# Kernel optimization log

Measured on AMD Instinct MI355X. Metric: run time of the kernel, lower is better.

The kernel has to match this reference:

```python
import jax, jax.numpy as jnp
import numpy as np

ALPHA = 0.2  # LeakyReLU negative slope


def setup_inputs() -> dict:
    key = jax.random.key(0)
    k1, k2, k3, k4 = jax.random.split(key, 4)
    B, W, N = 128, 128, 512  # batch, window_size, n_features
    x = jax.random.normal(k1, (B, W, N), dtype=jnp.float32)
    W_fc = jax.random.normal(k2, (W, W), dtype=jnp.float32) * (1.0 / np.sqrt(W))
    b_fc = jax.random.normal(k3, (W,), dtype=jnp.float32) * 0.01
    attn = jax.random.normal(k4, (2 * W, 1), dtype=jnp.float32) * (1.414 / np.sqrt(2 * W))
    return {"x": x, "W_fc": W_fc, "b_fc": b_fc, "attn": attn}


def reference(x, W_fc, b_fc, attn):
    # x: (B, window_size, n_features)
    Wsz = attn.shape[0] // 2
    xp = jnp.transpose(x, (0, 2, 1))                 # (B, N, W)
    h = jnp.einsum('bnw,vw->bnv', xp, W_fc) + b_fc   # fc over window dim: (B, N, W)
    # Split-projection equivalent of concat([x_i, h_j]) @ attn:
    a1 = attn[:Wsz, 0]
    a2 = attn[Wsz:, 0]
    s1 = xp @ a1                                     # (B, N) -- x_i part (repeat_interleave)
    s2 = h @ a2                                      # (B, N) -- h_j part (repeat)
    e = jax.nn.leaky_relu(s1[:, :, None] + s2[:, None, :], negative_slope=ALPHA)  # (B, N, N)
    attention = jax.nn.softmax(e, axis=2)            # softmax over j
    # dropout is identity in eval mode (train=False)
    out = jax.nn.sigmoid(jnp.einsum('bij,bjw->biw', attention, xp))  # (B, N, W)
    return jnp.transpose(out, (0, 2, 1))             # (B, W, N)
```

## Files before the change

kernel.cpp:

```cpp
#include <hip/hip_runtime.h>

#define Bb 128
#define Ww 128
#define Nn 512
#define ALPHA 0.2f
#define LOG2E 1.44269504088896340736f

typedef __attribute__((ext_vector_type(8))) short short8;
typedef __attribute__((ext_vector_type(4))) float f32x4;

__device__ __forceinline__ unsigned pk_bf16(float lo, float hi) {
  unsigned r;
  asm("v_cvt_pk_bf16_f32 %0, %1, %2" : "=v"(r) : "v"(lo), "v"(hi));
  return r;
}

__device__ __forceinline__ float v_exp2(float x) {
  float r;
  asm("v_exp_f32 %0, %1" : "=v"(r) : "v"(x));
  return r;
}

__device__ __forceinline__ float v_rcp(float x) {
  float r;
  asm("v_rcp_f32 %0, %1" : "=v"(r) : "v"(x));
  return r;
}

#define T_OFF   0
#define T_BYTES (64 * 129 * 8 * 2)
#define SR_OFF  (T_OFF + T_BYTES)
#define S1_OFF  (SR_OFF + 16384)
#define S2_OFF  (S1_OFF + 2048)
#define CV_OFF  (S2_OFF + 2048)
#define SMEM11  (CV_OFF + 528)

__launch_bounds__(512, 1)
__global__ void attn_f9(const float* __restrict__ x, const float* __restrict__ Wfc,
                        const float* __restrict__ bfc, const float* __restrict__ attn,
                        float* __restrict__ out) {
  extern __shared__ char smem[];
  ushort* tile = (ushort*)(smem + T_OFF);
  float*  sred = (float*)(smem + SR_OFF);
  float*  s1s  = (float*)(smem + S1_OFF);
  float*  s2s  = (float*)(smem + S2_OFF);
  float*  cvs  = (float*)(smem + CV_OFF);

  const int bid = blockIdx.x;
  const int xcd = bid & 7, idx = bid >> 3;
  const int b  = xcd * 16 + (idx >> 1);
  const int i0 = (idx & 1) * 256;
  const int t  = threadIdx.x;
  const int wv = t >> 6, lane = t & 63;
  const int wl = lane & 15, lg = lane >> 4;
  const float* xb = x + (size_t)b * (Ww * Nn);
  const int q = t & 63;

  {
    const int wcol = t & 127, vq = t >> 7;
    float p = 0.f;
#pragma unroll 8
    for (int vi = 0; vi < 32; ++vi) {
      const int v = vq * 32 + vi;
      p = fmaf(attn[Ww + v], Wfc[v * Ww + wcol], p);
    }
    sred[t] = p;
    if (t < 64) {
      float c0p = fmaf(bfc[t], attn[Ww + t], bfc[t + 64] * attn[Ww + 64 + t]);
#pragma unroll
      for (int off = 32; off; off >>= 1) c0p += __shfl_xor(c0p, off);
      if (t == 0) cvs[Ww] = c0p;
    }
  }
  __syncthreads();
  if (t < Ww) cvs[t] = sred[t] + sred[t + 128] + sred[t + 256] + sred[t + 384];
  __syncthreads();

  float s1p[8] = {0, 0, 0, 0, 0, 0, 0, 0};
  float s2p[8] = {0, 0, 0, 0, 0, 0, 0, 0};
  {
    float4 L0[16], L1[16];
#pragma unroll
    for (int k = 0; k < 16; ++k) {
      const float* s = xb + (size_t)(wv + 8 * k) * Nn + 8 * q;
      L0[k] = *reinterpret_cast<const float4*>(s);
      L1[k] = *reinterpret_cast<const float4*>(s + 4);
    }
#pragma unroll
    for (int k = 0; k < 16; ++k) {
      const int w = wv + 8 * k;
      const float aw = attn[w];
      const float cw = cvs[w];
      const float4 lo = L0[k], hi = L1[k];
      s1p[0] = fmaf(lo.x, aw, s1p[0]); s1p[1] = fmaf(lo.y, aw, s1p[1]);
      s1p[2] = fmaf(lo.z, aw, s1p[2]); s1p[3] = fmaf(lo.w, aw, s1p[3]);
      s1p[4] = fmaf(hi.x, aw, s1p[4]); s1p[5] = fmaf(hi.y, aw, s1p[5]);
      s1p[6] = fmaf(hi.z, aw, s1p[6]); s1p[7] = fmaf(hi.w, aw, s1p[7]);
      s2p[0] = fmaf(lo.x, cw, s2p[0]); s2p[1] = fmaf(lo.y, cw, s2p[1]);
      s2p[2] = fmaf(lo.z, cw, s2p[2]); s2p[3] = fmaf(lo.w, cw, s2p[3]);
      s2p[4] = fmaf(hi.x, cw, s2p[4]); s2p[5] = fmaf(hi.y, cw, s2p[5]);
      s2p[6] = fmaf(hi.z, cw, s2p[6]); s2p[7] = fmaf(hi.w, cw, s2p[7]);
      uint4 pk;
      pk.x = pk_bf16(lo.x, lo.y); pk.y = pk_bf16(lo.z, lo.w);
      pk.z = pk_bf16(hi.x, hi.y); pk.w = pk_bf16(hi.z, hi.w);
      *reinterpret_cast<uint4*>(tile + ((size_t)q * 129 + w) * 8) = pk;
    }
  }

  {
    f32x4* sv = reinterpret_cast<f32x4*>(&sred[t * 8]);
    sv[0] = (f32x4){s1p[0], s1p[1], s1p[2], s1p[3]};
    sv[1] = (f32x4){s1p[4], s1p[5], s1p[6], s1p[7]};
  }
  __syncthreads();
  float red;
  {
    float a = 0.f;
#pragma unroll
    for (int g = 0; g < 8; ++g) a += sred[((g * 64) + (t >> 3)) * 8 + (t & 7)];
    red = a;
  }
  __syncthreads();
  {
    s1s[t] = red * LOG2E;
    f32x4* sv = reinterpret_cast<f32x4*>(&sred[t * 8]);
    sv[0] = (f32x4){s2p[0], s2p[1], s2p[2], s2p[3]};
    sv[1] = (f32x4){s2p[4], s2p[5], s2p[6], s2p[7]};
  }
  __syncthreads();
  {
    float d = 0.f;
#pragma unroll
    for (int g = 0; g < 8; ++g) d += sred[((g * 64) + (t >> 3)) * 8 + (t & 7)];
    s2s[t] = (d + cvs[Ww]) * LOG2E;
  }
  __syncthreads();

  float s1i[2];
  s1i[0] = s1s[i0 + wv * 32 + wl];
  s1i[1] = s1s[i0 + wv * 32 + 16 + wl];

  f32x4 acc[2][8];
  f32x4 accl[2];
#pragma unroll
  for (int a = 0; a < 2; ++a) {
    accl[a] = (f32x4){0.f, 0.f, 0.f, 0.f};
#pragma unroll
    for (int f = 0; f < 8; ++f) acc[a][f] = (f32x4){0.f, 0.f, 0.f, 0.f};
  }
  short8 ones;
#pragma unroll
  for (int e = 0; e < 8; ++e) ones[e] = (short)0x3F80;

  for (int jj = 0; jj < 16; ++jj) {
    const int jb = jj * 32 + 8 * lg;
    float sv[8];
    *reinterpret_cast<float4*>(&sv[0]) = *reinterpret_cast<const float4*>(&s2s[jb]);
    *reinterpret_cast<float4*>(&sv[4]) = *reinterpret_cast<const float4*>(&s2s[jb + 4]);
    float p0[8], p1[8];
#pragma unroll
    for (int e = 0; e < 8; ++e) {
      const float u0 = s1i[0] + sv[e];
      p0[e] = v_exp2(fmaxf(u0, ALPHA * u0));
      const float u1 = s1i[1] + sv[e];
      p1[e] = v_exp2(fmaxf(u1, ALPHA * u1));
    }
    short8 af0, af1;
    unsigned* a0u = reinterpret_cast<unsigned*>(&af0);
    unsigned* a1u = reinterpret_cast<unsigned*>(&af1);
    a0u[0] = pk_bf16(p0[0], p0[1]); a0u[1] = pk_bf16(p0[2], p0[3]);
    a0u[2] = pk_bf16(p0[4], p0[5]); a0u[3] = pk_bf16(p0[6], p0[7]);
    a1u[0] = pk_bf16(p1[0], p1[1]); a1u[1] = pk_bf16(p1[2], p1[3]);
    a1u[2] = pk_bf16(p1[4], p1[5]); a1u[3] = pk_bf16(p1[6], p1[7]);

    const ushort* tb = tile + (size_t)(jj * 4 + lg) * 129 * 8;
#pragma unroll
    for (int f = 0; f < 8; ++f) {
      const short8 bfr = *reinterpret_cast<const short8*>(tb + (16 * f + wl) * 8);
      acc[0][f] = __builtin_amdgcn_mfma_f32_16x16x32_bf16(af0, bfr, acc[0][f], 0, 0, 0);
      acc[1][f] = __builtin_amdgcn_mfma_f32_16x16x32_bf16(af1, bfr, acc[1][f], 0, 0, 0);
    }
    accl[0] = __builtin_amdgcn_mfma_f32_16x16x32_bf16(af0, ones, accl[0], 0, 0, 0);
    accl[1] = __builtin_amdgcn_mfma_f32_16x16x32_bf16(af1, ones, accl[1], 0, 0, 0);
  }

  float* outb = out + (size_t)b * (Ww * Nn);
#pragma unroll
  for (int a = 0; a < 2; ++a) {
    float invl[4];
#pragma unroll
    for (int m = 0; m < 4; ++m) invl[m] = LOG2E * v_rcp(accl[a][m]);
    const int ibase = i0 + wv * 32 + 16 * a + lg * 4;
#pragma unroll
    for (int f = 0; f < 8; ++f) {
      float4 o;
      o.x = v_rcp(1.f + v_exp2(-(acc[a][f][0] * invl[0])));
      o.y = v_rcp(1.f + v_exp2(-(acc[a][f][1] * invl[1])));
      o.z = v_rcp(1.f + v_exp2(-(acc[a][f][2] * invl[2])));
      o.w = v_rcp(1.f + v_exp2(-(acc[a][f][3] * invl[3])));
      *reinterpret_cast<float4*>(outb + (16 * f + wl) * Nn + ibase) = o;
    }
  }
}

extern "C" void kernel_launch(void* const* d_in, const int* in_sizes, int n_in,
                              void* d_out, int out_size, void* d_ws, size_t ws_size,
                              hipStream_t stream) {
  const float* x    = (const float*)d_in[0];
  const float* Wfc  = (const float*)d_in[1];
  const float* bfc  = (const float*)d_in[2];
  const float* attn = (const float*)d_in[3];
  float* out = (float*)d_out;

  (void)hipFuncSetAttribute(reinterpret_cast<const void*>(&attn_f9),
                            hipFuncAttributeMaxDynamicSharedMemorySize, SMEM11);
  attn_f9<<<256, 512, SMEM11, stream>>>(x, Wfc, bfc, attn, out);
}
```

Baseline: 28.07 us.

## Double block size to 1024 threads, one 16-row tile per wave

The block grows from 8 to 16 waves. Each wave now computes a single 16-row MFMA tile instead of two, and the staging, transposition and reduction phases are re-split so each thread loads one float4 per row instead of two. The aim is more wave-level parallelism and latency hiding per CU, plus fewer registers per thread. The cost is more barrier participants, half the A-fragment reuse per LDS B-fragment load (doubling LDS read traffic), and 8-byte instead of 16-byte tile writes.

Result: faster. 26.38 us (-6.0%).

```diff
diff --git a/kernel.cpp b/kernel.cpp
--- a/kernel.cpp
+++ b/kernel.cpp
@@ -33,12 +33,12 @@
 #define S1_OFF  (SR_OFF + 16384)
 #define S2_OFF  (S1_OFF + 2048)
 #define CV_OFF  (S2_OFF + 2048)
-#define SMEM11  (CV_OFF + 528)
+#define SMEM12  (CV_OFF + 528)
 
-__launch_bounds__(512, 1)
-__global__ void attn_f9(const float* __restrict__ x, const float* __restrict__ Wfc,
-                        const float* __restrict__ bfc, const float* __restrict__ attn,
-                        float* __restrict__ out) {
+__launch_bounds__(1024, 1)
+__global__ void attn_k(const float* __restrict__ x, const float* __restrict__ Wfc,
+                       const float* __restrict__ bfc, const float* __restrict__ attn,
+                       float* __restrict__ out) {
   extern __shared__ char smem[];
   ushort* tile = (ushort*)(smem + T_OFF);
   float*  sred = (float*)(smem + SR_OFF);
@@ -51,17 +51,19 @@
   const int b  = xcd * 16 + (idx >> 1);
   const int i0 = (idx & 1) * 256;
   const int t  = threadIdx.x;
-  const int wv = t >> 6, lane = t & 63;
+  const int wvw = t >> 6;
+  const int lane = t & 63;
   const int wl = lane & 15, lg = lane >> 4;
+  const int g  = t >> 7;
+  const int q2 = t & 127;
   const float* xb = x + (size_t)b * (Ww * Nn);
-  const int q = t & 63;
 
   {
     const int wcol = t & 127, vq = t >> 7;
     float p = 0.f;
-#pragma unroll 8
-    for (int vi = 0; vi < 32; ++vi) {
-      const int v = vq * 32 + vi;
+#pragma unroll
+    for (int vi = 0; vi < 16; ++vi) {
+      const int v = vq * 16 + vi;
       p = fmaf(attn[Ww + v], Wfc[v * Ww + wcol], p);
     }
     sred[t] = p;
@@ -73,81 +75,63 @@
     }
   }
   __syncthreads();
-  if (t < Ww) cvs[t] = sred[t] + sred[t + 128] + sred[t + 256] + sred[t + 384];
+  if (t < Ww) {
+    float s = 0.f;
+#pragma unroll
+    for (int j = 0; j < 8; ++j) s += sred[t + 128 * j];
+    cvs[t] = s;
+  }
   __syncthreads();
 
-  float s1p[8] = {0, 0, 0, 0, 0, 0, 0, 0};
-  float s2p[8] = {0, 0, 0, 0, 0, 0, 0, 0};
+  float s1p[4] = {0.f, 0.f, 0.f, 0.f};
+  float s2p[4] = {0.f, 0.f, 0.f, 0.f};
   {
-    float4 L0[16], L1[16];
+    float4 L[16];
+#pragma unroll
+    for (int k = 0; k < 16; ++k)
+      L[k] = *reinterpret_cast<const float4*>(xb + (size_t)(g + 8 * k) * Nn + 4 * q2);
 #pragma unroll
     for (int k = 0; k < 16; ++k) {
-      const float* s = xb + (size_t)(wv + 8 * k) * Nn + 8 * q;
-      L0[k] = *reinterpret_cast<const float4*>(s);
-      L1[k] = *reinterpret_cast<const float4*>(s + 4);
-    }
-#pragma unroll
-    for (int k = 0; k < 16; ++k) {
-      const int w = wv + 8 * k;
+      const int w = g + 8 * k;
       const float aw = attn[w];
       const float cw = cvs[w];
-      const float4 lo = L0[k], hi = L1[k];
-      s1p[0] = fmaf(lo.x, aw, s1p[0]); s1p[1] = fmaf(lo.y, aw, s1p[1]);
-      s1p[2] = fmaf(lo.z, aw, s1p[2]); s1p[3] = fmaf(lo.w, aw, s1p[3]);
-      s1p[4] = fmaf(hi.x, aw, s1p[4]); s1p[5] = fmaf(hi.y, aw, s1p[5]);
-      s1p[6] = fmaf(hi.z, aw, s1p[6]); s1p[7] = fmaf(hi.w, aw, s1p[7]);
-      s2p[0] = fmaf(lo.x, cw, s2p[0]); s2p[1] = fmaf(lo.y, cw, s2p[1]);
-      s2p[2] = fmaf(lo.z, cw, s2p[2]); s2p[3] = fmaf(lo.w, cw, s2p[3]);
-      s2p[4] = fmaf(hi.x, cw, s2p[4]); s2p[5] = fmaf(hi.y, cw, s2p[5]);
-      s2p[6] = fmaf(hi.z, cw, s2p[6]); s2p[7] = fmaf(hi.w, cw, s2p[7]);
-      uint4 pk;
-      pk.x = pk_bf16(lo.x, lo.y); pk.y = pk_bf16(lo.z, lo.w);
-      pk.z = pk_bf16(hi.x, hi.y); pk.w = pk_bf16(hi.z, hi.w);
-      *reinterpret_cast<uint4*>(tile + ((size_t)q * 129 + w) * 8) = pk;
+      const float4 v = L[k];
+      s1p[0] = fmaf(v.x, aw, s1p[0]); s1p[1] = fmaf(v.y, aw, s1p[1]);
+      s1p[2] = fmaf(v.z, aw, s1p[2]); s1p[3] = fmaf(v.w, aw, s1p[3]);
+      s2p[0] = fmaf(v.x, cw, s2p[0]); s2p[1] = fmaf(v.y, cw, s2p[1]);
+      s2p[2] = fmaf(v.z, cw, s2p[2]); s2p[3] = fmaf(v.w, cw, s2p[3]);
+      uint2 pk;
+      pk.x = pk_bf16(v.x, v.y);
+      pk.y = pk_bf16(v.z, v.w);
+      *reinterpret_cast<uint2*>(tile + ((size_t)(q2 >> 1) * 129 + w) * 8 + (q2 & 1) * 4) = pk;
     }
   }
 
-  {
-    f32x4* sv = reinterpret_cast<f32x4*>(&sred[t * 8]);
-    sv[0] = (f32x4){s1p[0], s1p[1], s1p[2], s1p[3]};
-    sv[1] = (f32x4){s1p[4], s1p[5], s1p[6], s1p[7]};
+  *reinterpret_cast<f32x4*>(&sred[t * 4]) = (f32x4){s1p[0], s1p[1], s1p[2], s1p[3]};
+  __syncthreads();
+  float red = 0.f;
+  if (t < 512) {
+#pragma unroll
+    for (int j = 0; j < 8; ++j) red += sred[j * 512 + t];
   }
   __syncthreads();
-  float red;
-  {
-    float a = 0.f;
-#pragma unroll
-    for (int g = 0; g < 8; ++g) a += sred[((g * 64) + (t >> 3)) * 8 + (t & 7)];
-    red = a;
-  }
+  if (t < 512) s1s[t] = red * LOG2E;
+  *reinterpret_cast<f32x4*>(&sred[t * 4]) = (f32x4){s2p[0], s2p[1], s2p[2], s2p[3]};
   __syncthreads();
-  {
-    s1s[t] = red * LOG2E;
-    f32x4* sv = reinterpret_cast<f32x4*>(&sred[t * 8]);
-    sv[0] = (f32x4){s2p[0], s2p[1], s2p[2], s2p[3]};
-    sv[1] = (f32x4){s2p[4], s2p[5], s2p[6], s2p[7]};
-  }
-  __syncthreads();
-  {
+  if (t < 512) {
     float d = 0.f;
 #pragma unroll
-    for (int g = 0; g < 8; ++g) d += sred[((g * 64) + (t >> 3)) * 8 + (t & 7)];
+    for (int j = 0; j < 8; ++j) d += sred[j * 512 + t];
     s2s[t] = (d + cvs[Ww]) * LOG2E;
   }
   __syncthreads();
 
-  float s1i[2];
-  s1i[0] = s1s[i0 + wv * 32 + wl];
-  s1i[1] = s1s[i0 + wv * 32 + 16 + wl];
+  const float s1i = s1s[i0 + wvw * 16 + wl];
 
-  f32x4 acc[2][8];
-  f32x4 accl[2];
+  f32x4 acc[8];
+  f32x4 accl = (f32x4){0.f, 0.f, 0.f, 0.f};
 #pragma unroll
-  for (int a = 0; a < 2; ++a) {
-    accl[a] = (f32x4){0.f, 0.f, 0.f, 0.f};
-#pragma unroll
-    for (int f = 0; f < 8; ++f) acc[a][f] = (f32x4){0.f, 0.f, 0.f, 0.f};
-  }
+  for (int f = 0; f < 8; ++f) acc[f] = (f32x4){0.f, 0.f, 0.f, 0.f};
   short8 ones;
 #pragma unroll
   for (int e = 0; e < 8; ++e) ones[e] = (short)0x3F80;
@@ -157,49 +141,39 @@
     float sv[8];
     *reinterpret_cast<float4*>(&sv[0]) = *reinterpret_cast<const float4*>(&s2s[jb]);
     *reinterpret_cast<float4*>(&sv[4]) = *reinterpret_cast<const float4*>(&s2s[jb + 4]);
-    float p0[8], p1[8];
+    float p[8];
 #pragma unroll
     for (int e = 0; e < 8; ++e) {
-      const float u0 = s1i[0] + sv[e];
-      p0[e] = v_exp2(fmaxf(u0, ALPHA * u0));
-      const float u1 = s1i[1] + sv[e];
-      p1[e] = v_exp2(fmaxf(u1, ALPHA * u1));
+      const float u = s1i + sv[e];
+      p[e] = v_exp2(fmaxf(u, ALPHA * u));
     }
-    short8 af0, af1;
-    unsigned* a0u = reinterpret_cast<unsigned*>(&af0);
-    unsigned* a1u = reinterpret_cast<unsigned*>(&af1);
-    a0u[0] = pk_bf16(p0[0], p0[1]); a0u[1] = pk_bf16(p0[2], p0[3]);
-    a0u[2] = pk_bf16(p0[4], p0[5]); a0u[3] = pk_bf16(p0[6], p0[7]);
-    a1u[0] = pk_bf16(p1[0], p1[1]); a1u[1] = pk_bf16(p1[2], p1[3]);
-    a1u[2] = pk_bf16(p1[4], p1[5]); a1u[3] = pk_bf16(p1[6], p1[7]);
+    short8 af;
+    unsigned* au = reinterpret_cast<unsigned*>(&af);
+    au[0] = pk_bf16(p[0], p[1]); au[1] = pk_bf16(p[2], p[3]);
+    au[2] = pk_bf16(p[4], p[5]); au[3] = pk_bf16(p[6], p[7]);
 
     const ushort* tb = tile + (size_t)(jj * 4 + lg) * 129 * 8;
 #pragma unroll
     for (int f = 0; f < 8; ++f) {
       const short8 bfr = *reinterpret_cast<const short8*>(tb + (16 * f + wl) * 8);
-      acc[0][f] = __builtin_amdgcn_mfma_f32_16x16x32_bf16(af0, bfr, acc[0][f], 0, 0, 0);
-      acc[1][f] = __builtin_amdgcn_mfma_f32_16x16x32_bf16(af1, bfr, acc[1][f], 0, 0, 0);
+      acc[f] = __builtin_amdgcn_mfma_f32_16x16x32_bf16(af, bfr, acc[f], 0, 0, 0);
     }
-    accl[0] = __builtin_amdgcn_mfma_f32_16x16x32_bf16(af0, ones, accl[0], 0, 0, 0);
-    accl[1] = __builtin_amdgcn_mfma_f32_16x16x32_bf16(af1, ones, accl[1], 0, 0, 0);
+    accl = __builtin_amdgcn_mfma_f32_16x16x32_bf16(af, ones, accl, 0, 0, 0);
   }
 
+  float invl[4];
+#pragma unroll
+  for (int m = 0; m < 4; ++m) invl[m] = LOG2E * v_rcp(accl[m]);
+  const int ibase = i0 + wvw * 16 + lg * 4;
   float* outb = out + (size_t)b * (Ww * Nn);
 #pragma unroll
-  for (int a = 0; a < 2; ++a) {
-    float invl[4];
-#pragma unroll
-    for (int m = 0; m < 4; ++m) invl[m] = LOG2E * v_rcp(accl[a][m]);
-    const int ibase = i0 + wv * 32 + 16 * a + lg * 4;
-#pragma unroll
-    for (int f = 0; f < 8; ++f) {
-      float4 o;
-      o.x = v_rcp(1.f + v_exp2(-(acc[a][f][0] * invl[0])));
-      o.y = v_rcp(1.f + v_exp2(-(acc[a][f][1] * invl[1])));
-      o.z = v_rcp(1.f + v_exp2(-(acc[a][f][2] * invl[2])));
-      o.w = v_rcp(1.f + v_exp2(-(acc[a][f][3] * invl[3])));
-      *reinterpret_cast<float4*>(outb + (16 * f + wl) * Nn + ibase) = o;
-    }
+  for (int f = 0; f < 8; ++f) {
+    float4 o;
+    o.x = v_rcp(1.f + v_exp2(-(acc[f][0] * invl[0])));
+    o.y = v_rcp(1.f + v_exp2(-(acc[f][1] * invl[1])));
+    o.z = v_rcp(1.f + v_exp2(-(acc[f][2] * invl[2])));
+    o.w = v_rcp(1.f + v_exp2(-(acc[f][3] * invl[3])));
+    *reinterpret_cast<float4*>(outb + (16 * f + wl) * Nn + ibase) = o;
   }
 }
 
@@ -212,7 +186,7 @@
   const float* attn = (const float*)d_in[3];
   float* out = (float*)d_out;
 
-  (void)hipFuncSetAttribute(reinterpret_cast<const void*>(&attn_f9),
-                            hipFuncAttributeMaxDynamicSharedMemorySize, SMEM11);
-  attn_f9<<<256, 512, SMEM11, stream>>>(x, Wfc, bfc, attn, out);
+  (void)hipFuncSetAttribute(reinterpret_cast<const void*>(&attn_k),
+                            hipFuncAttributeMaxDynamicSharedMemorySize, SMEM12);
+  attn_k<<<256, 1024, SMEM12, stream>>>(x, Wfc, bfc, attn, out);
 }
```
